# Kernel tuning notes

Hardware: AMD Instinct MI355X
Metric: run time of the kernel (lower is better)

The kernel has to match this reference:

```python
import jax, jax.numpy as jnp
import numpy as np
import math

ALPHA = math.exp(-0.001 * 1000.0)  # exp(-dt * tau_filter_inv)
T, B, D_IN, D_OUT = 2048, 32, 512, 512


def setup_inputs() -> dict:
    key = jax.random.key(0)
    k1, k2, k3 = jax.random.split(key, 3)
    bound = 1.0 / math.sqrt(D_IN)  # torch Linear default init range
    return {
        "input_tensor": jax.random.normal(k1, (T, B, D_IN), dtype=jnp.float32),
        "weight": jax.random.uniform(k2, (D_OUT, D_IN), minval=-bound, maxval=bound, dtype=jnp.float32),
        "bias": jax.random.uniform(k3, (D_OUT,), minval=-bound, maxval=bound, dtype=jnp.float32),
    }


def reference(input_tensor, weight, bias):
    # y[t] = W x[t] + b   -> [T, B, D_OUT]
    y = jnp.einsum("tbi,oi->tbo", input_tensor, weight) + bias
    alpha = jnp.asarray(ALPHA, dtype=y.dtype)

    # out[0] = y[0]; out[t] = alpha * out[t-1] + y[t]
    def step(carry, yt):
        out = alpha * carry + yt
        return out, out

    _, rest = jax.lax.scan(step, y[0], y[1:])
    return jnp.concatenate([y[:1], rest], axis=0)
```

## Files before the change

kernel.cpp:

```cpp
#include <hip/hip_runtime.h>
#include <stdint.h>

#define T_DIM 2048
#define B_DIM 32
#define DIN   512
#define DOUT  512
#define M_DIM (T_DIM * B_DIM)
#define COLS  (B_DIM * DIN)
#define COLS4 (COLS / 4)

#define ALPHA_F 0.36787944117144233f
#define INV_1MA 1.5819767068693265f

#define FT_T    32
#define FT_HALO 8
#define FT_ROWS (FT_T + FT_HALO)
#define FT_C4   64

#define FCHUNKS  32
#define FCHUNK_T 64
#define FHALO    16

typedef float  floatx4 __attribute__((ext_vector_type(4)));
typedef __bf16 bf16x8  __attribute__((ext_vector_type(8)));

__device__ __forceinline__ uint32_t pk2(float a, float b) {
  uint32_t ua = __float_as_uint(a); ua += 0x7fffu + ((ua >> 16) & 1u);
  uint32_t ub = __float_as_uint(b); ub += 0x7fffu + ((ub >> 16) & 1u);
  return (ua >> 16) | (ub & 0xffff0000u);
}

__device__ __forceinline__ void gload_lds16(const void* g, void* lds) {
  __builtin_amdgcn_global_load_lds(
      (const __attribute__((address_space(1))) void*)g,
      (__attribute__((address_space(3))) void*)lds,
      16, 0, 0);
}

__device__ __forceinline__ void fma4(float4& c, const float4& v) {
  c.x = fmaf(ALPHA_F, c.x, v.x);
  c.y = fmaf(ALPHA_F, c.y, v.y);
  c.z = fmaf(ALPHA_F, c.z, v.z);
  c.w = fmaf(ALPHA_F, c.w, v.w);
}

__global__ void wconv_kernel(const float* __restrict__ W,
                             uint16_t* __restrict__ WB)
{
  const int t = blockIdx.x * 256 + threadIdx.x;
  const float4* W4 = (const float4*)W;
#pragma unroll
  for (int j = 0; j < 8; ++j) {
    const int b4 = t * 16 + j * 2;
    float4 w0 = W4[b4], w1 = W4[b4 + 1];
    uint4 p;
    p.x = pk2(w0.x, w0.y); p.y = pk2(w0.z, w0.w);
    p.z = pk2(w1.x, w1.y); p.w = pk2(w1.z, w1.w);
    *(uint4*)&WB[t * 64 + j * 8] = p;
  }
}

__global__ void filter_x_kernel(const float* __restrict__ X,
                                uint16_t* __restrict__ XF)
{
  __shared__ __align__(16) float lds[FT_ROWS * FT_C4 * 4];

  const int ct = blockIdx.x;
  const int tt = blockIdx.y;
  const int tid  = threadIdx.x;
  const int lane = tid & 63;
  const int w    = tid >> 6;
  const int t0   = tt * FT_T;
  const size_t gc4 = (size_t)ct * FT_C4;

  float4* L4 = (float4*)lds;

  if (tt == 0) {
    const float4 z = {0.0f, 0.0f, 0.0f, 0.0f};
#pragma unroll
    for (int i = 0; i < 2; ++i)
      L4[tid + i * 256] = z;
#pragma unroll
    for (int i = 0; i < 8; ++i) {
      const int row = 8 + w + i * 4;
      gload_lds16(X + ((size_t)(t0 + row - 8) * COLS4 + gc4 + lane) * 4,
                  &L4[row * FT_C4]);
    }
  } else {
#pragma unroll
    for (int i = 0; i < 10; ++i) {
      const int row = w + i * 4;
      gload_lds16(X + ((size_t)(t0 - 8 + row) * COLS4 + gc4 + lane) * 4,
                  &L4[row * FT_C4]);
    }
  }
  __syncthreads();

  const int seg = w;
  float4 carry = {0.0f, 0.0f, 0.0f, 0.0f};
#pragma unroll
  for (int j = 0; j < 16; ++j) {
    const int r = seg * 8 + j;
    float4 v = L4[r * FT_C4 + lane];
    fma4(carry, v);
    if (j >= 8) {
      const int o = seg * 8 + j - 8;
      uint2 p;
      p.x = pk2(carry.x, carry.y);
      p.y = pk2(carry.z, carry.w);
      *(uint2*)&XF[((size_t)(t0 + o) * COLS4 + gc4 + lane) * 4] = p;
    }
  }
}

__launch_bounds__(256, 4)
__global__ void gemm_bf16_kernel(const uint16_t* __restrict__ XF,
                                 const uint16_t* __restrict__ WB,
                                 const float* __restrict__ bias,
                                 float* __restrict__ Y)
{
  __shared__ __align__(16) uint16_t As[128 * 64];
  __shared__ __align__(16) uint16_t Bs[128 * 64];

  const int bid = blockIdx.x;
  const int lg = (bid & 7) * 256 + (bid >> 3);
  const int n0 = (lg & 3) * 128;
  const int m0 = (lg >> 2) * 128;

  const int tid  = threadIdx.x;
  const int lane = tid & 63;
  const int w    = tid >> 6;
  const int r    = lane & 15;
  const int q    = lane >> 4;
  const int wm   = w >> 1;
  const int wn   = w & 1;

  const int srow_base = w * 32 + (lane >> 3);
  const int schunk    = lane & 7;

  floatx4 acc[4][4];
#pragma unroll
  for (int i = 0; i < 4; ++i)
#pragma unroll
    for (int j = 0; j < 4; ++j) {
      floatx4 z = {0.0f, 0.0f, 0.0f, 0.0f};
      acc[i][j] = z;
    }

  for (int kt = 0; kt < DIN / 64; ++kt) {
    const int k0 = kt * 64;
#pragma unroll
    for (int i = 0; i < 4; ++i) {
      const int row = srow_base + i * 8;
      const int sc = schunk ^ (row & 7);
      gload_lds16(XF + (size_t)(m0 + row) * DIN + k0 + sc * 8,
                  &As[(w * 32 + i * 8) * 64]);
      gload_lds16(WB + (size_t)(n0 + row) * DIN + k0 + sc * 8,
                  &Bs[(w * 32 + i * 8) * 64]);
    }
    __syncthreads();

#pragma unroll
    for (int kk = 0; kk < 2; ++kk) {
      bf16x8 af[4], bfr[4];
#pragma unroll
      for (int mi = 0; mi < 4; ++mi) {
        const int row = wm * 64 + mi * 16 + r;
        const int cch = (kk * 4 + q) ^ (row & 7);
        af[mi] = *(const bf16x8*)&As[row * 64 + (cch << 3)];
      }
#pragma unroll
      for (int ni = 0; ni < 4; ++ni) {
        const int row = wn * 64 + ni * 16 + r;
        const int cch = (kk * 4 + q) ^ (row & 7);
        bfr[ni] = *(const bf16x8*)&Bs[row * 64 + (cch << 3)];
      }
#pragma unroll
      for (int mi = 0; mi < 4; ++mi)
#pragma unroll
        for (int ni = 0; ni < 4; ++ni)
          acc[mi][ni] = __builtin_amdgcn_mfma_f32_16x16x32_bf16(
              af[mi], bfr[ni], acc[mi][ni], 0, 0, 0);
    }
    __syncthreads();
  }

#pragma unroll
  for (int mi = 0; mi < 4; ++mi) {
    const int rowb = m0 + wm * 64 + mi * 16;
    const int t = rowb >> 5;
    const float s = (1.0f - __expf(-(float)(t + 1))) * INV_1MA;
#pragma unroll
    for (int ni = 0; ni < 4; ++ni) {
      const int col = n0 + wn * 64 + ni * 16 + r;
      const float sb = s * bias[col];
#pragma unroll
      for (int j = 0; j < 4; ++j)
        Y[(size_t)(rowb + q * 4 + j) * DOUT + col] = acc[mi][ni][j] + sb;
    }
  }
}

__launch_bounds__(256, 2)
__global__ void gemm_bias_kernel(const float* __restrict__ X,
                                 const float* __restrict__ W,
                                 const float* __restrict__ bias,
                                 float* __restrict__ Y,
                                 float* __restrict__ halo,
                                 int halo_on)
{
  __shared__ __align__(16) uint16_t As[128 * 64];
  __shared__ __align__(16) uint16_t Bsh[128 * 64];

  const int tid  = threadIdx.x;
  const int lane = tid & 63;
  const int wave = tid >> 6;
  const int wm   = wave >> 1;
  const int wn   = wave & 1;
  const int r    = lane & 15;
  const int q    = lane >> 4;

  const int m0 = blockIdx.y * 128;
  const int n0 = blockIdx.x * 128;

  floatx4 acc[4][4];
#pragma unroll
  for (int i = 0; i < 4; ++i)
#pragma unroll
    for (int j = 0; j < 4; ++j) {
      floatx4 z = {0.0f, 0.0f, 0.0f, 0.0f};
      acc[i][j] = z;
    }

  for (int kt = 0; kt < DIN / 64; ++kt) {
    const int k0 = kt * 64;
#pragma unroll
    for (int j = 0; j < 4; ++j) {
      const int cid = tid + j * 256;
      const int row = cid >> 3;
      const int c   = cid & 7;
      const int slot = (c ^ (row & 7)) << 3;

      const float* ga = &X[(size_t)(m0 + row) * DIN + k0 + c * 8];
      float4 a0 = *(const float4*)ga;
      float4 a1 = *(const float4*)(ga + 4);
      uint4 pa;
      pa.x = pk2(a0.x, a0.y); pa.y = pk2(a0.z, a0.w);
      pa.z = pk2(a1.x, a1.y); pa.w = pk2(a1.z, a1.w);
      *(uint4*)&As[row * 64 + slot] = pa;

      const float* gb = &W[(size_t)(n0 + row) * DIN + k0 + c * 8];
      float4 b0 = *(const float4*)gb;
      float4 b1 = *(const float4*)(gb + 4);
      uint4 pb;
      pb.x = pk2(b0.x, b0.y); pb.y = pk2(b0.z, b0.w);
      pb.z = pk2(b1.x, b1.y); pb.w = pk2(b1.z, b1.w);
      *(uint4*)&Bsh[row * 64 + slot] = pb;
    }
    __syncthreads();

#pragma unroll
    for (int kk = 0; kk < 2; ++kk) {
      bf16x8 af[4], bfr[4];
#pragma unroll
      for (int mi = 0; mi < 4; ++mi) {
        const int row = wm * 64 + mi * 16 + r;
        const int c   = (kk * 4 + q) ^ (row & 7);
        af[mi] = *(const bf16x8*)&As[row * 64 + (c << 3)];
      }
#pragma unroll
      for (int ni = 0; ni < 4; ++ni) {
        const int row = wn * 64 + ni * 16 + r;
        const int c   = (kk * 4 + q) ^ (row & 7);
        bfr[ni] = *(const bf16x8*)&Bsh[row * 64 + (c << 3)];
      }
#pragma unroll
      for (int mi = 0; mi < 4; ++mi)
#pragma unroll
        for (int ni = 0; ni < 4; ++ni)
          acc[mi][ni] = __builtin_amdgcn_mfma_f32_16x16x32_bf16(
              af[mi], bfr[ni], acc[mi][ni], 0, 0, 0);
    }
    __syncthreads();
  }

#pragma unroll
  for (int ni = 0; ni < 4; ++ni) {
    const int col = n0 + wn * 64 + ni * 16 + r;
    const float bv = bias[col];
#pragma unroll
    for (int mi = 0; mi < 4; ++mi) {
      const int rowm = m0 + wm * 64 + mi * 16 + q * 4;
      const int t = rowm >> 5;
      const int b = rowm & 31;
      const int tloc = t & (FCHUNK_T - 1);
      const bool hw = halo_on && (tloc >= FCHUNK_T - FHALO) && (t < T_DIM - FCHUNK_T);
      const size_t hbase = hw
          ? ((size_t)(((t >> 6) + 1) * FHALO + (tloc - (FCHUNK_T - FHALO))) * COLS)
          : 0;
#pragma unroll
      for (int j = 0; j < 4; ++j) {
        const float v = acc[mi][ni][j] + bv;
        Y[(size_t)(rowm + j) * DOUT + col] = v;
        if (hw) halo[hbase + (size_t)(b + j) * DOUT + col] = v;
      }
    }
  }
}

__global__ void scan_kernel(float* __restrict__ Y,
                            const float* __restrict__ halo,
                            int chunk_len)
{
  const int col4 = blockIdx.x * blockDim.x + threadIdx.x;
  const int c = blockIdx.y;

  float4* Y4 = (float4*)Y;
  const float4* H4 = (const float4*)halo;

  float4 carry = {0.0f, 0.0f, 0.0f, 0.0f};
  if (c > 0) {
#pragma unroll
    for (int h = 0; h < FHALO; ++h) {
      float4 v = H4[(size_t)(c * FHALO + h) * COLS4 + col4];
      fma4(carry, v);
    }
  }

  size_t idx = (size_t)c * chunk_len * COLS4 + col4;
  float4 ynext = Y4[idx];
  for (int t = 0; t < chunk_len; ++t) {
    float4 y = ynext;
    if (t + 1 < chunk_len) ynext = Y4[idx + COLS4];
    fma4(carry, y);
    Y4[idx] = carry;
    idx += COLS4;
  }
}

extern "C" void kernel_launch(void* const* d_in, const int* in_sizes, int n_in,
                              void* d_out, int out_size, void* d_ws, size_t ws_size,
                              hipStream_t stream)
{
  const float* X    = (const float*)d_in[0];
  const float* W    = (const float*)d_in[1];
  const float* bias = (const float*)d_in[2];
  float* Y = (float*)d_out;

  const size_t need_new = (size_t)M_DIM * DIN * 2 + (size_t)DOUT * DIN * 2;

  if (ws_size >= need_new) {
    uint16_t* XF = (uint16_t*)d_ws;
    uint16_t* WB = XF + (size_t)M_DIM * DIN;

    wconv_kernel<<<16, 256, 0, stream>>>(W, WB);
    dim3 gf(COLS4 / FT_C4, T_DIM / FT_T);
    filter_x_kernel<<<gf, 256, 0, stream>>>(X, XF);
    gemm_bf16_kernel<<<2048, 256, 0, stream>>>(XF, WB, bias, Y);
  } else {
    float* halo = (float*)d_ws;
    const size_t halo_need = (size_t)FCHUNKS * FHALO * COLS * sizeof(float);
    const int halo_on = (ws_size >= halo_need) ? 1 : 0;

    dim3 g1(DOUT / 128, M_DIM / 128);
    gemm_bias_kernel<<<g1, 256, 0, stream>>>(X, W, bias, Y, halo, halo_on);

    const int n_chunks = halo_on ? FCHUNKS : 1;
    dim3 g2(COLS4 / 256, n_chunks);
    scan_kernel<<<g2, 256, 0, stream>>>(Y, halo, T_DIM / n_chunks);
  }
}
```

Before: 91.38 us.

## Restructure input filter into long per-wave time runs with double-buffered loads

The filter kernel now gives each wave 64 consecutive time steps instead of 8. It reads only an 8-row halo once at the start, then streams 8-row sub-tiles through a double LDS buffer, loading the next tile while the current one is filtered. This cuts redundant halo reads of X and overlaps loads with compute. In exchange the grid shrinks from 4096 to 512 blocks and each wave keeps only 8 rows in flight, which may reduce memory-level parallelism and adds a barrier per sub-tile.

```diff
diff --git a/kernel.cpp b/kernel.cpp
--- a/kernel.cpp
+++ b/kernel.cpp
@@ -12,10 +12,10 @@
 #define ALPHA_F 0.36787944117144233f
 #define INV_1MA 1.5819767068693265f
 
-#define FT_T    32
-#define FT_HALO 8
-#define FT_ROWS (FT_T + FT_HALO)
 #define FT_C4   64
+#define FT_WT   64
+#define FT_BT   256
+#define FT_NSUB 8
 
 #define FCHUNKS  32
 #define FCHUNK_T 64
@@ -63,53 +63,60 @@
 __global__ void filter_x_kernel(const float* __restrict__ X,
                                 uint16_t* __restrict__ XF)
 {
-  __shared__ __align__(16) float lds[FT_ROWS * FT_C4 * 4];
+  __shared__ __align__(16) float4 buf[2][32 * FT_C4];
 
   const int ct = blockIdx.x;
-  const int tt = blockIdx.y;
+  const int tb = blockIdx.y * FT_BT;
   const int tid  = threadIdx.x;
   const int lane = tid & 63;
   const int w    = tid >> 6;
-  const int t0   = tt * FT_T;
-  const size_t gc4 = (size_t)ct * FT_C4;
-
-  float4* L4 = (float4*)lds;
-
-  if (tt == 0) {
+  const int tw   = tb + w * FT_WT;
+  const size_t gc4 = (size_t)ct * FT_C4 + lane;
+
+  const float4* X4 = (const float4*)X;
+
+  if (tb == 0 && w == 0) {
     const float4 z = {0.0f, 0.0f, 0.0f, 0.0f};
 #pragma unroll
-    for (int i = 0; i < 2; ++i)
-      L4[tid + i * 256] = z;
-#pragma unroll
-    for (int i = 0; i < 8; ++i) {
-      const int row = 8 + w + i * 4;
-      gload_lds16(X + ((size_t)(t0 + row - 8) * COLS4 + gc4 + lane) * 4,
-                  &L4[row * FT_C4]);
-    }
+    for (int r = 0; r < 8; ++r) buf[0][r * FT_C4 + lane] = z;
   } else {
 #pragma unroll
-    for (int i = 0; i < 10; ++i) {
-      const int row = w + i * 4;
-      gload_lds16(X + ((size_t)(t0 - 8 + row) * COLS4 + gc4 + lane) * 4,
-                  &L4[row * FT_C4]);
-    }
-  }
+    for (int r = 0; r < 8; ++r)
+      gload_lds16(&X4[(size_t)(tw - 8 + r) * COLS4 + gc4],
+                  &buf[0][(w * 8 + r) * FT_C4]);
+  }
+
+#pragma unroll
+  for (int r = 0; r < 8; ++r)
+    gload_lds16(&X4[(size_t)(tw + r) * COLS4 + gc4],
+                &buf[1][(w * 8 + r) * FT_C4]);
+
   __syncthreads();
 
-  const int seg = w;
   float4 carry = {0.0f, 0.0f, 0.0f, 0.0f};
 #pragma unroll
-  for (int j = 0; j < 16; ++j) {
-    const int r = seg * 8 + j;
-    float4 v = L4[r * FT_C4 + lane];
-    fma4(carry, v);
-    if (j >= 8) {
-      const int o = seg * 8 + j - 8;
+  for (int r = 0; r < 8; ++r) fma4(carry, buf[0][(w * 8 + r) * FT_C4 + lane]);
+
+  int cur = 1;
+#pragma unroll
+  for (int j = 0; j < FT_NSUB; ++j) {
+    if (j + 1 < FT_NSUB) {
+#pragma unroll
+      for (int r = 0; r < 8; ++r)
+        gload_lds16(&X4[(size_t)(tw + (j + 1) * 8 + r) * COLS4 + gc4],
+                    &buf[cur ^ 1][(w * 8 + r) * FT_C4]);
+    }
+#pragma unroll
+    for (int r = 0; r < 8; ++r) {
+      float4 v = buf[cur][(w * 8 + r) * FT_C4 + lane];
+      fma4(carry, v);
       uint2 p;
       p.x = pk2(carry.x, carry.y);
       p.y = pk2(carry.z, carry.w);
-      *(uint2*)&XF[((size_t)(t0 + o) * COLS4 + gc4 + lane) * 4] = p;
-    }
+      *(uint2*)&XF[((size_t)(tw + j * 8 + r) * COLS4 + gc4) * 4] = p;
+    }
+    __syncthreads();
+    cur ^= 1;
   }
 }
 
@@ -354,7 +361,7 @@
     uint16_t* WB = XF + (size_t)M_DIM * DIN;
 
     wconv_kernel<<<16, 256, 0, stream>>>(W, WB);
-    dim3 gf(COLS4 / FT_C4, T_DIM / FT_T);
+    dim3 gf(COLS4 / FT_C4, T_DIM / FT_BT);
     filter_x_kernel<<<gf, 256, 0, stream>>>(X, XF);
     gemm_bf16_kernel<<<2048, 256, 0, stream>>>(XF, WB, bias, Y);
   } else {
```

Result: slower. 104.6 us (+14.5%).
